# Performance work log

Measured on AMD Instinct MI355X. Metric: run time of the kernel, lower is better.

## Reference

```python
import jax, jax.numpy as jnp
import numpy as np

T = 256          # trellis length (steps per sequence)
L = 16           # state bits
K = 2            # code bits per step
V = 2            # weights emitted per step
TLUT_BITS = 10   # LUT index bits
OUT, IN = 4096, 4096
NSEQ = (OUT * IN) // (T * V)      # 32768
CODES_PER_WORD = 32 // K          # 16


def fwht(x):
    """Normalized fast Walsh-Hadamard transform along the last axis (power-of-2)."""
    n = x.shape[-1]
    lead = x.shape[:-1]
    h = 1
    while h < n:
        x = x.reshape(lead + (n // (2 * h), 2, h))
        a, b = x[..., 0, :], x[..., 1, :]
        x = jnp.stack([a + b, a - b], axis=-2).reshape(lead + (n,))
        h *= 2
    return x / jnp.sqrt(jnp.asarray(n, x.dtype))


def decode_trellis(trellis, tlut):
    """Bit-unpack K-bit transition codes, run the L-bit shift-register trellis,
    and look up V weight values per state in the LUT."""
    t = jnp.arange(T)
    words = trellis[:, t // CODES_PER_WORD]            # [NSEQ, T] int32
    shifts = (32 - K) - K * (t % CODES_PER_WORD)       # MSB-first unpack
    codes = (words >> shifts) & (2 ** K - 1)           # [NSEQ, T]

    def step(state, code):
        state = ((state << K) | code) & (2 ** L - 1)
        return state, state

    _, states = jax.lax.scan(step, jnp.zeros(trellis.shape[0], jnp.int32),
                             codes.T.astype(jnp.int32))  # states: [T, NSEQ]
    states = states.T                                   # [NSEQ, T]
    vals = tlut[states & (2 ** TLUT_BITS - 1)]          # [NSEQ, T, V] LUT gather
    return vals.reshape(OUT, IN)


def incoherence_process(w_hat, SU, SV):
    """W = diag(SV) H_out  W_hat  H_in diag(SU)  (random-sign Hadamard)."""
    w = fwht(w_hat)        # Hadamard along in-dim
    w = fwht(w.T).T        # Hadamard along out-dim
    return w * SV[:, None] * SU[None, :]


def setup_inputs() -> dict:
    key = jax.random.key(0)
    ks = jax.random.split(key, 5)
    x = jax.random.normal(ks[0], (8192, IN), jnp.float32)
    trellis = jax.random.randint(ks[1], (NSEQ, 32 * T * K // (32 * 32)) if False else (NSEQ, (T * K) // 32), 0, 2147483647, dtype=jnp.int32)
    tlut = jax.random.normal(ks[2], (2 ** TLUT_BITS, V), jnp.float32)
    SU = jnp.sign(jax.random.normal(ks[3], (IN,), jnp.float32)) * 0.02
    SV = jnp.sign(jax.random.normal(ks[4], (OUT,), jnp.float32)) * 0.02
    return {"x": x, "trellis": trellis, "tlut": tlut, "SU": SU, "SV": SV}


def reference(x, trellis, tlut, SU, SV):
    w_hat = decode_trellis(trellis, tlut)       # [OUT, IN] dequantized weight
    w = incoherence_process(w_hat, SU, SV)      # Hadamard incoherence undo
    return x @ w.T                              # F.linear
```

## Files before the change

kernel.cpp:

```cpp
#include <hip/hip_runtime.h>
#include <hip/hip_bf16.h>
#include <stdint.h>

typedef __bf16 bf16x8 __attribute__((ext_vector_type(8)));
typedef float  f32x4  __attribute__((ext_vector_type(4)));

#define IN_DIM  4096
#define OUT_DIM 4096
#define M_DIM   8192

#define AS1 __attribute__((address_space(1)))
#define AS3 __attribute__((address_space(3)))

static __device__ __forceinline__ void gload_lds16(const void* g, void* l) {
  __builtin_amdgcn_global_load_lds((const AS1 void*)g, (AS3 void*)l, 16, 0, 0);
}
static __device__ __forceinline__ float bf2f(unsigned short u) {
  union { uint32_t i; float f; } c; c.i = (uint32_t)u << 16; return c.f;
}
static __device__ __forceinline__ unsigned short f2bf(float f) {
  __hip_bfloat16 h = __float2bfloat16(f); return *(const unsigned short*)&h;
}

__global__ __launch_bounds__(256) void k_decode_fwht_row(
    const int* __restrict__ trellis, const float2* __restrict__ tlut,
    const float* __restrict__ SU, __hip_bfloat16* __restrict__ w)
{
  __shared__ float buf[4096];
  __shared__ int words[128];
  __shared__ float2 lut[1024];
  const int tid = threadIdx.x;
  const int r = blockIdx.x;

  if (tid < 128) words[tid] = trellis[r * 128 + tid];
  for (int i = tid; i < 1024; i += 256) lut[i] = tlut[i];
  __syncthreads();

  {
    const int t  = tid;
    const int wi = t >> 4;
    const int sh = 30 - 2 * (t & 15);
    const unsigned mask = (t < 4) ? ((1u << (2 * t + 2)) - 1u) : 1023u;
    #pragma unroll
    for (int s = 0; s < 8; ++s) {
      unsigned lo = (unsigned)words[s * 16 + wi];
      unsigned hi = wi ? (unsigned)words[s * 16 + wi - 1] : 0u;
      unsigned long long comb = ((unsigned long long)hi << 32) | (unsigned long long)lo;
      unsigned st = ((unsigned)(comb >> sh)) & mask;
      float2 v = lut[st];
      buf[s * 512 + 2 * t]     = v.x + v.y;
      buf[s * 512 + 2 * t + 1] = v.x - v.y;
    }
  }
  __syncthreads();

  for (int h = 2; h < 4096; h <<= 1) {
    #pragma unroll
    for (int q = 0; q < 8; ++q) {
      int b = q * 256 + tid;
      int i = ((b & ~(h - 1)) << 1) | (b & (h - 1));
      float a = buf[i], c = buf[i + h];
      buf[i]     = a + c;
      buf[i + h] = a - c;
    }
    __syncthreads();
  }

  for (int it2 = 0; it2 < 2; ++it2) {
    int c0 = (it2 * 256 + tid) * 8;
    union { unsigned short us[8]; uint4 v; } p;
    #pragma unroll
    for (int e = 0; e < 8; ++e)
      p.us[e] = f2bf(buf[c0 + e] * SU[c0 + e] * 0.015625f);
    *(uint4*)(w + (size_t)r * IN_DIM + c0) = p.v;
  }
}

__global__ __launch_bounds__(256) void k_fwht64_lo(__hip_bfloat16* __restrict__ w)
{
  __shared__ float tile[64][65];
  const int tid = threadIdx.x;
  const int rb = blockIdx.y, cb = blockIdx.x;

  for (int it = 0; it < 2; ++it) {
    int chunk = it * 256 + tid;
    int rr = chunk >> 3, jc = chunk & 7;
    uint4 v = *(const uint4*)(w + (size_t)(rb * 64 + rr) * IN_DIM + cb * 64 + jc * 8);
    const unsigned short* u = (const unsigned short*)&v;
    #pragma unroll
    for (int e = 0; e < 8; ++e) tile[rr][jc * 8 + e] = bf2f(u[e]);
  }
  __syncthreads();

  const int c = tid & 63, qf = tid >> 6;
  for (int h = 1; h < 64; h <<= 1) {
    #pragma unroll
    for (int u = 0; u < 8; ++u) {
      int b = qf * 8 + u;
      int i = ((b & ~(h - 1)) << 1) | (b & (h - 1));
      float a = tile[i][c], d = tile[i + h][c];
      tile[i][c]     = a + d;
      tile[i + h][c] = a - d;
    }
    __syncthreads();
  }

  for (int it = 0; it < 2; ++it) {
    int chunk = it * 256 + tid;
    int rr = chunk >> 3, jc = chunk & 7;
    union { unsigned short us[8]; uint4 v; } p;
    #pragma unroll
    for (int e = 0; e < 8; ++e) p.us[e] = f2bf(tile[rr][jc * 8 + e]);
    *(uint4*)(w + (size_t)(rb * 64 + rr) * IN_DIM + cb * 64 + jc * 8) = p.v;
  }
}

__global__ __launch_bounds__(256) void k_fwht64_hi(__hip_bfloat16* __restrict__ w,
                                                   const float* __restrict__ SV)
{
  __shared__ float tile[64][65];
  const int tid = threadIdx.x;
  const int r0 = blockIdx.y, cb = blockIdx.x;

  for (int it = 0; it < 2; ++it) {
    int chunk = it * 256 + tid;
    int r1 = chunk >> 3, jc = chunk & 7;
    uint4 v = *(const uint4*)(w + (size_t)(r0 + 64 * r1) * IN_DIM + cb * 64 + jc * 8);
    const unsigned short* u = (const unsigned short*)&v;
    #pragma unroll
    for (int e = 0; e < 8; ++e) tile[r1][jc * 8 + e] = bf2f(u[e]);
  }
  __syncthreads();

  const int c = tid & 63, qf = tid >> 6;
  for (int h = 1; h < 64; h <<= 1) {
    #pragma unroll
    for (int u = 0; u < 8; ++u) {
      int b = qf * 8 + u;
      int i = ((b & ~(h - 1)) << 1) | (b & (h - 1));
      float a = tile[i][c], d = tile[i + h][c];
      tile[i][c]     = a + d;
      tile[i + h][c] = a - d;
    }
    __syncthreads();
  }

  for (int it = 0; it < 2; ++it) {
    int chunk = it * 256 + tid;
    int r1 = chunk >> 3, jc = chunk & 7;
    int row = r0 + 64 * r1;
    float sv = SV[row] * 0.015625f;
    union { unsigned short us[8]; uint4 v; } p;
    #pragma unroll
    for (int e = 0; e < 8; ++e) p.us[e] = f2bf(tile[r1][jc * 8 + e] * sv);
    *(uint4*)(w + (size_t)row * IN_DIM + cb * 64 + jc * 8) = p.v;
  }
}

__global__ __launch_bounds__(256) void k_cvt_x(const float* __restrict__ x,
                                               __hip_bfloat16* __restrict__ xb)
{
  size_t i = ((size_t)blockIdx.x * 256 + threadIdx.x) * 8;
  float4 v0 = *(const float4*)(x + i);
  float4 v1 = *(const float4*)(x + i + 4);
  union { __hip_bfloat16 h[8]; uint4 u; } p;
  p.h[0] = __float2bfloat16(v0.x); p.h[1] = __float2bfloat16(v0.y);
  p.h[2] = __float2bfloat16(v0.z); p.h[3] = __float2bfloat16(v0.w);
  p.h[4] = __float2bfloat16(v1.x); p.h[5] = __float2bfloat16(v1.y);
  p.h[6] = __float2bfloat16(v1.z); p.h[7] = __float2bfloat16(v1.w);
  *(uint4*)(xb + i) = p.u;
}

#define GBM 256
#define GBN 256
#define GBK 64
#define NT  (IN_DIM / GBK)

__global__ __launch_bounds__(512, 2) void k_gemm256(
    const __hip_bfloat16* __restrict__ X,
    const __hip_bfloat16* __restrict__ W,
    float* __restrict__ out)
{
  extern __shared__ __hip_bfloat16 smem[];
  __hip_bfloat16* As = smem;
  __hip_bfloat16* Bs = smem + 2 * 16384;

  const int tid  = threadIdx.x;
  const int lane = tid & 63;
  const int wave = tid >> 6;
  const int wm   = wave >> 2;
  const int wn   = wave & 3;
  const int lm   = lane & 15;
  const int lq   = lane >> 4;
  const int s_rw = tid >> 3;
  const int s_jj = tid & 7;

  const int nwg  = gridDim.x * gridDim.y;
  const int cpx  = nwg >> 3;
  const int orig = blockIdx.y * gridDim.x + blockIdx.x;
  const int swz  = (orig & 7) * cpx + (orig >> 3);
  const int bx   = swz % gridDim.x;
  const int by   = swz / gridDim.x;
  const int m0 = by * GBM, n0 = bx * GBN;

  f32x4 acc[8][4] = {};

#define STAGE_A(buf, u, kt) do {                                              \
    int row_ = (u) * 64 + s_rw;                                               \
    int js_  = s_jj ^ (row_ & 7);                                             \
    gload_lds16(X + (size_t)(m0 + row_) * IN_DIM + (kt) * GBK + js_ * 8,      \
                As + (buf) * 16384 + row_ * 64 + s_jj * 8);                   \
  } while (0)
#define STAGE_BE(buf, half, kt) do {                                          \
    int row_ = (half) * 128 + (s_rw & 31) + ((s_rw & 32) << 1);               \
    int js_  = s_jj ^ (row_ & 7);                                             \
    gload_lds16(W + (size_t)(n0 + row_) * IN_DIM + (kt) * GBK + js_ * 8,      \
                Bs + (buf) * 16384 + row_ * 64 + s_jj * 8);                   \
  } while (0)
#define STAGE_BL(buf, half, kt) do {                                          \
    int row_ = (half) * 128 + 32 + (s_rw & 31) + ((s_rw & 32) << 1);          \
    int js_  = s_jj ^ (row_ & 7);                                             \
    gload_lds16(W + (size_t)(n0 + row_) * IN_DIM + (kt) * GBK + js_ * 8,      \
                Bs + (buf) * 16384 + row_ * 64 + s_jj * 8);                   \
  } while (0)

#define RD_A_TO(DST, QM, BUF) do {                                            \
    const __hip_bfloat16* Ab_ = As + (BUF) * 16384;                           \
    _Pragma("unroll")                                                         \
    for (int mi2 = 0; mi2 < 4; ++mi2) {                                       \
      int r_ = wm * 128 + (QM) * 64 + mi2 * 16 + lm;                          \
      _Pragma("unroll")                                                       \
      for (int kk = 0; kk < 2; ++kk) {                                        \
        int q_ = kk * 4 + lq;                                                 \
        DST[mi2][kk] = *(const bf16x8*)(Ab_ + r_ * 64 + ((q_ ^ (r_ & 7)) << 3)); \
      }                                                                       \
    }                                                                         \
  } while (0)
#define RD_B_TO(DST, QN, BUF) do {                                            \
    const __hip_bfloat16* Bb_ = Bs + (BUF) * 16384;                           \
    _Pragma("unroll")                                                         \
    for (int ni2 = 0; ni2 < 2; ++ni2) {                                       \
      int r_ = wn * 64 + (QN) * 32 + ni2 * 16 + lm;                           \
      _Pragma("unroll")                                                       \
      for (int kk = 0; kk < 2; ++kk) {                                        \
        int q_ = kk * 4 + lq;                                                 \
        DST[ni2][kk] = *(const bf16x8*)(Bb_ + r_ * 64 + ((q_ ^ (r_ & 7)) << 3)); \
      }                                                                       \
    }                                                                         \
  } while (0)

#define FENCE asm volatile("" ::: "memory")
#define PH_BAR do { FENCE; __builtin_amdgcn_s_barrier(); FENCE;               \
                    __builtin_amdgcn_s_setprio(1); } while (0)
#define MFMA_Q2(QM, QN, AF, BF) do {                                          \
    _Pragma("unroll")                                                         \
    for (int mi2 = 0; mi2 < 4; ++mi2)                                         \
      _Pragma("unroll")                                                       \
      for (int ni2 = 0; ni2 < 2; ++ni2)                                       \
        _Pragma("unroll")                                                     \
        for (int kk = 0; kk < 2; ++kk)                                        \
          acc[(QM) * 4 + mi2][(QN) * 2 + ni2] =                               \
              __builtin_amdgcn_mfma_f32_16x16x32_bf16(                        \
                  AF[mi2][kk], BF[ni2][kk],                                   \
                  acc[(QM) * 4 + mi2][(QN) * 2 + ni2], 0, 0, 0);              \
  } while (0)
#define VM4 do { asm volatile("s_waitcnt vmcnt(4)" ::: "memory"); } while (0)
#define PH_END    do { __builtin_amdgcn_s_setprio(0); FENCE;                  \
                       __builtin_amdgcn_s_barrier(); FENCE; } while (0)
#define PH_END_VM do { __builtin_amdgcn_s_setprio(0); VM4;                    \
                       __builtin_amdgcn_s_barrier(); FENCE; } while (0)

  STAGE_BE(0, 0, 0); STAGE_BE(0, 1, 0);
  STAGE_A (0, 0, 0); STAGE_A (0, 2, 0);
  STAGE_BL(0, 0, 0); STAGE_BL(0, 1, 0);
  STAGE_A (0, 1, 0); STAGE_A (0, 3, 0);
  STAGE_A (1, 0, 1); STAGE_A (1, 2, 1);
  STAGE_BL(1, 0, 1); STAGE_BL(1, 1, 1);
  asm volatile("s_waitcnt vmcnt(4)" ::: "memory");
  __builtin_amdgcn_s_barrier(); FENCE;

  for (int it = 0; it < NT / 2; ++it) {
    const int t1 = 2 * it + 1;
    const int t2 = (2 * it + 2 < NT) ? 2 * it + 2 : NT - 1;
    const int t3 = (2 * it + 3 < NT) ? 2 * it + 3 : NT - 1;

    bf16x8 aE[4][2], aO[4][2], b0[2][2], b1[2][2];
    bf16x8 aE1[4][2], aO1[4][2], b01[2][2], b11[2][2];

    RD_A_TO(aE, 0, 0); RD_B_TO(b0, 0, 0);
    STAGE_A(1, 1, t1); STAGE_A(1, 3, t1);
    PH_BAR; MFMA_Q2(0, 0, aE, b0); PH_END;
    RD_B_TO(b1, 1, 0);
    STAGE_BE(1, 0, t1); STAGE_BE(1, 1, t1);
    PH_BAR; MFMA_Q2(0, 1, aE, b1); PH_END;
    RD_A_TO(aO, 1, 0);
    STAGE_A(0, 0, t2); STAGE_A(0, 2, t2);
    PH_BAR; MFMA_Q2(1, 1, aO, b1); PH_END;
    STAGE_BL(0, 0, t2); STAGE_BL(0, 1, t2);
    PH_BAR; MFMA_Q2(1, 0, aO, b0); PH_END_VM;

    RD_A_TO(aE1, 0, 1); RD_B_TO(b01, 0, 1);
    STAGE_A(0, 1, t2); STAGE_A(0, 3, t2);
    PH_BAR; MFMA_Q2(0, 0, aE1, b01); PH_END;
    RD_B_TO(b11, 1, 1);
    STAGE_BE(0, 0, t2); STAGE_BE(0, 1, t2);
    PH_BAR; MFMA_Q2(0, 1, aE1, b11); PH_END;
    RD_A_TO(aO1, 1, 1);
    STAGE_A(1, 0, t3); STAGE_A(1, 2, t3);
    PH_BAR; MFMA_Q2(1, 1, aO1, b11); PH_END;
    STAGE_BL(1, 0, t3); STAGE_BL(1, 1, t3);
    PH_BAR; MFMA_Q2(1, 0, aO1, b01); PH_END_VM;
  }

  #pragma unroll
  for (int mi = 0; mi < 8; ++mi) {
    #pragma unroll
    for (int ni = 0; ni < 4; ++ni) {
      int col   = n0 + wn * 64 + ni * 16 + lm;
      int rbase = m0 + wm * 128 + mi * 16 + lq * 4;
      #pragma unroll
      for (int rg = 0; rg < 4; ++rg) {
        out[(size_t)(rbase + rg) * OUT_DIM + col] = acc[mi][ni][rg];
      }
    }
  }
#undef PH_END_VM
#undef PH_END
#undef VM4
#undef MFMA_Q2
#undef PH_BAR
#undef FENCE
#undef RD_B_TO
#undef RD_A_TO
#undef STAGE_BL
#undef STAGE_BE
#undef STAGE_A
}

extern "C" void kernel_launch(void* const* d_in, const int* in_sizes, int n_in,
                              void* d_out, int out_size, void* d_ws, size_t ws_size,
                              hipStream_t stream) {
  (void)in_sizes; (void)n_in; (void)out_size; (void)ws_size;
  const float* x       = (const float*)d_in[0];
  const int*   trellis = (const int*)d_in[1];
  const float* tlut    = (const float*)d_in[2];
  const float* SU      = (const float*)d_in[3];
  const float* SV      = (const float*)d_in[4];
  float* out = (float*)d_out;

  __hip_bfloat16* Wd = (__hip_bfloat16*)d_ws;
  __hip_bfloat16* Xb = (__hip_bfloat16*)((char*)d_ws + (size_t)32 * 1024 * 1024);

  k_decode_fwht_row<<<4096, 256, 0, stream>>>(trellis, (const float2*)tlut, SU, Wd);
  k_fwht64_lo<<<dim3(64, 64), 256, 0, stream>>>(Wd);
  k_fwht64_hi<<<dim3(64, 64), 256, 0, stream>>>(Wd, SV);
  k_cvt_x<<<16384, 256, 0, stream>>>(x, Xb);

  hipFuncSetAttribute((const void*)k_gemm256,
                      hipFuncAttributeMaxDynamicSharedMemorySize, 131072);
  k_gemm256<<<dim3(IN_DIM / GBN, M_DIM / GBM), 512, 131072, stream>>>(Xb, Wd, out);
}
```

Before: 355.0 us.

## Software-pipeline LDS fragment reads one phase ahead of MFMA in GEMM loop

```diff
diff --git a/kernel.cpp b/kernel.cpp
--- a/kernel.cpp
+++ b/kernel.cpp
@@ -250,8 +250,8 @@
   } while (0)
 
 #define FENCE asm volatile("" ::: "memory")
-#define PH_BAR do { FENCE; __builtin_amdgcn_s_barrier(); FENCE;               \
-                    __builtin_amdgcn_s_setprio(1); } while (0)
+#define BAR do { FENCE; __builtin_amdgcn_s_barrier(); FENCE; } while (0)
+#define VM4 do { asm volatile("s_waitcnt vmcnt(4)" ::: "memory"); } while (0)
 #define MFMA_Q2(QM, QN, AF, BF) do {                                          \
     _Pragma("unroll")                                                         \
     for (int mi2 = 0; mi2 < 4; ++mi2)                                         \
@@ -264,11 +264,8 @@
                   AF[mi2][kk], BF[ni2][kk],                                   \
                   acc[(QM) * 4 + mi2][(QN) * 2 + ni2], 0, 0, 0);              \
   } while (0)
-#define VM4 do { asm volatile("s_waitcnt vmcnt(4)" ::: "memory"); } while (0)
-#define PH_END    do { __builtin_amdgcn_s_setprio(0); FENCE;                  \
-                       __builtin_amdgcn_s_barrier(); FENCE; } while (0)
-#define PH_END_VM do { __builtin_amdgcn_s_setprio(0); VM4;                    \
-                       __builtin_amdgcn_s_barrier(); FENCE; } while (0)
+
+  bf16x8 aE0[4][2], b00a[2][2];
 
   STAGE_BE(0, 0, 0); STAGE_BE(0, 1, 0);
   STAGE_A (0, 0, 0); STAGE_A (0, 2, 0);
@@ -276,41 +273,79 @@
   STAGE_A (0, 1, 0); STAGE_A (0, 3, 0);
   STAGE_A (1, 0, 1); STAGE_A (1, 2, 1);
   STAGE_BL(1, 0, 1); STAGE_BL(1, 1, 1);
-  asm volatile("s_waitcnt vmcnt(4)" ::: "memory");
-  __builtin_amdgcn_s_barrier(); FENCE;
+  STAGE_A (1, 1, 1); STAGE_A (1, 3, 1);
+  asm volatile("s_waitcnt vmcnt(6)" ::: "memory");
+  BAR;
+  RD_A_TO(aE0, 0, 0); RD_B_TO(b00a, 0, 0);
 
   for (int it = 0; it < NT / 2; ++it) {
     const int t1 = 2 * it + 1;
     const int t2 = (2 * it + 2 < NT) ? 2 * it + 2 : NT - 1;
     const int t3 = (2 * it + 3 < NT) ? 2 * it + 3 : NT - 1;
 
-    bf16x8 aE[4][2], aO[4][2], b0[2][2], b1[2][2];
-    bf16x8 aE1[4][2], aO1[4][2], b01[2][2], b11[2][2];
-
-    RD_A_TO(aE, 0, 0); RD_B_TO(b0, 0, 0);
-    STAGE_A(1, 1, t1); STAGE_A(1, 3, t1);
-    PH_BAR; MFMA_Q2(0, 0, aE, b0); PH_END;
-    RD_B_TO(b1, 1, 0);
+    bf16x8 aO0[4][2], aE1[4][2], aO1[4][2];
+    bf16x8 b10[2][2], b00b[2][2], b01a[2][2], b11[2][2], b01b[2][2];
+
+    BAR;
     STAGE_BE(1, 0, t1); STAGE_BE(1, 1, t1);
-    PH_BAR; MFMA_Q2(0, 1, aE, b1); PH_END;
-    RD_A_TO(aO, 1, 0);
+    __builtin_amdgcn_s_setprio(1);
+    RD_B_TO(b10, 1, 0);
+    MFMA_Q2(0, 0, aE0, b00a);
+    __builtin_amdgcn_s_setprio(0);
+
+    BAR;
     STAGE_A(0, 0, t2); STAGE_A(0, 2, t2);
-    PH_BAR; MFMA_Q2(1, 1, aO, b1); PH_END;
+    __builtin_amdgcn_s_setprio(1);
+    RD_A_TO(aO0, 1, 0);
+    MFMA_Q2(0, 1, aE0, b10);
+    __builtin_amdgcn_s_setprio(0);
+
+    BAR;
     STAGE_BL(0, 0, t2); STAGE_BL(0, 1, t2);
-    PH_BAR; MFMA_Q2(1, 0, aO, b0); PH_END_VM;
-
-    RD_A_TO(aE1, 0, 1); RD_B_TO(b01, 0, 1);
+    __builtin_amdgcn_s_setprio(1);
+    RD_B_TO(b00b, 0, 0);
+    MFMA_Q2(1, 1, aO0, b10);
+    __builtin_amdgcn_s_setprio(0);
+    VM4;
+
+    BAR;
     STAGE_A(0, 1, t2); STAGE_A(0, 3, t2);
-    PH_BAR; MFMA_Q2(0, 0, aE1, b01); PH_END;
+    __builtin_amdgcn_s_setprio(1);
+    RD_A_TO(aE1, 0, 1); RD_B_TO(b01a, 0, 1);
+    MFMA_Q2(1, 0, aO0, b00b);
+    __builtin_amdgcn_s_setprio(0);
+
+    BAR;
+    STAGE_BE(0, 0, t2); STAGE_BE(0, 1, t2);
+    __builtin_amdgcn_s_setprio(1);
     RD_B_TO(b11, 1, 1);
-    STAGE_BE(0, 0, t2); STAGE_BE(0, 1, t2);
-    PH_BAR; MFMA_Q2(0, 1, aE1, b11); PH_END;
+    MFMA_Q2(0, 0, aE1, b01a);
+    __builtin_amdgcn_s_setprio(0);
+
+    BAR;
+    STAGE_A(1, 0, t3); STAGE_A(1, 2, t3);
+    __builtin_amdgcn_s_setprio(1);
     RD_A_TO(aO1, 1, 1);
-    STAGE_A(1, 0, t3); STAGE_A(1, 2, t3);
-    PH_BAR; MFMA_Q2(1, 1, aO1, b11); PH_END;
+    MFMA_Q2(0, 1, aE1, b11);
+    __builtin_amdgcn_s_setprio(0);
+
+    BAR;
     STAGE_BL(1, 0, t3); STAGE_BL(1, 1, t3);
-    PH_BAR; MFMA_Q2(1, 0, aO1, b01); PH_END_VM;
-  }
+    __builtin_amdgcn_s_setprio(1);
+    RD_B_TO(b01b, 0, 1);
+    MFMA_Q2(1, 1, aO1, b11);
+    __builtin_amdgcn_s_setprio(0);
+    VM4;
+
+    BAR;
+    STAGE_A(1, 1, t3); STAGE_A(1, 3, t3);
+    __builtin_amdgcn_s_setprio(1);
+    RD_A_TO(aE0, 0, 0); RD_B_TO(b00a, 0, 0);
+    MFMA_Q2(1, 0, aO1, b01b);
+    __builtin_amdgcn_s_setprio(0);
+  }
+
+  asm volatile("s_waitcnt vmcnt(0)" ::: "memory");
 
   #pragma unroll
   for (int mi = 0; mi < 8; ++mi) {
@@ -324,11 +359,9 @@
       }
     }
   }
-#undef PH_END_VM
-#undef PH_END
+#undef MFMA_Q2
 #undef VM4
-#undef MFMA_Q2
-#undef PH_BAR
+#undef BAR
 #undef FENCE
 #undef RD_B_TO
 #undef RD_A_TO
```

Result: faster. 346.1 us (-2.5%).
